# Kernel tuning notes

Measured on AMD Instinct MI355X. Metric: run time of the kernel, lower is better.

## Reference

```python
import jax, jax.numpy as jnp
import numpy as np

B, TU, TZ, V, H, E = 64, 128, 16, 32000, 512, 256
EPS = 1e-10


def setup_inputs() -> dict:
    key = jax.random.key(0)
    ks = jax.random.split(key, 22)
    s = 0.02  # weight init scale
    inp = {
        "embed_z": jax.random.normal(ks[0], (1, B, E), jnp.float32),
        "last_hidden": jax.random.normal(ks[1], (1, B, H), jnp.float32),
        "u_enc_out": jax.random.normal(ks[2], (TU, B, H), jnp.float32),
        # previous-turn z posterior: rows are probability distributions over vocab
        "pv_pz_proba": jax.nn.softmax(jax.random.normal(ks[3], (TZ, B, V), jnp.float32), axis=-1),
        "pv_z_dec_out": jax.random.normal(ks[4], (TZ, B, H), jnp.float32),
        "rand_eps": jax.random.normal(ks[5], (B, E), jnp.float32),
        "u_input_np": jax.random.randint(ks[6], (TU, B), 0, V),
        "u_input": jax.random.randint(ks[6], (TU, B), 0, V),   # unused by forward
        "m_input_np": jax.random.randint(ks[7], (TU, B), 0, V),  # unused by forward
        # GRU (single layer, single step)
        "W_ih": jax.random.normal(ks[8], (3 * H, E), jnp.float32) * s,
        "W_hh": jax.random.normal(ks[9], (3 * H, H), jnp.float32) * s,
        "b_ih": jnp.zeros((3 * H,), jnp.float32),
        "b_hh": jnp.zeros((3 * H,), jnp.float32),
        # w1: hidden -> vocab
        "W_w1": jax.random.normal(ks[10], (V, H), jnp.float32) * s,
        "b_w1": jnp.zeros((V,), jnp.float32),
        # proj_copy1 / proj_copy2: hidden -> hidden
        "W_p1": jax.random.normal(ks[11], (H, H), jnp.float32) * s,
        "b_p1": jnp.zeros((H,), jnp.float32),
        "W_p2": jax.random.normal(ks[12], (H, H), jnp.float32) * s,
        "b_p2": jnp.zeros((H,), jnp.float32),
        # mu / log_sigma: vocab -> embed
        "W_mu": jax.random.normal(ks[13], (E, V), jnp.float32) * s,
        "b_mu": jnp.zeros((E,), jnp.float32),
        "W_ls": jax.random.normal(ks[14], (E, V), jnp.float32) * s,
        "b_ls": jnp.zeros((E,), jnp.float32),
    }
    return inp


def reference(embed_z, last_hidden, u_enc_out, pv_pz_proba, pv_z_dec_out, rand_eps,
              u_input_np, u_input, m_input_np,
              W_ih, W_hh, b_ih, b_hh, W_w1, b_w1, W_p1, b_p1, W_p2, b_p2,
              W_mu, b_mu, W_ls, b_ls):
    # --- single GRU step (dropout is identity at rate 0 / eval) ---
    x = embed_z[0]          # (B,E)
    h0 = last_hidden[0]     # (B,H)
    gi = x @ W_ih.T + b_ih
    gh = h0 @ W_hh.T + b_hh
    i_r, i_z, i_n = jnp.split(gi, 3, axis=1)
    h_r, h_z, h_n = jnp.split(gh, 3, axis=1)
    r = jax.nn.sigmoid(i_r + h_r)
    z = jax.nn.sigmoid(i_z + h_z)
    n = jnp.tanh(i_n + r * h_n)
    h = (1.0 - z) * n + z * h0              # (B,H) == gru_out.squeeze(0)

    gen_score = h @ W_w1.T + b_w1           # (B,V)

    # --- user copy score (force_stable path): stable exp + scatter-add by token id ---
    uc = jnp.tanh(jnp.swapaxes(u_enc_out, 0, 1) @ W_p1.T + b_p1)   # (B,TU,H)
    us = jnp.einsum('bth,bh->bt', uc, h)                            # (B,TU)
    um = jnp.max(us, axis=1, keepdims=True)
    ue = jnp.exp(us - um)
    tok = u_input_np.T                                              # (B,TU)
    # sparse one-hot bmm == 1e-10 * sum_t e  +  scatter-add of e into vocab bin tok (tok!=0)
    scat = jnp.zeros((B, V), us.dtype).at[jnp.arange(B)[:, None], tok].add(
        ue * (tok != 0))
    u_copy = jnp.log(EPS * jnp.sum(ue, axis=1, keepdims=True) + scat) + um  # (B,V)

    # --- previous-z copy score (exp path taken when force_stable) ---
    # shift: drop last step, prepend 1e-10 fill
    shifted = jnp.concatenate(
        [jnp.full((1, B, V), EPS, pv_pz_proba.dtype), pv_pz_proba[:-1]], axis=0)  # (TZ,B,V)
    pc = jnp.tanh(jnp.swapaxes(pv_z_dec_out, 0, 1) @ W_p2.T + b_p2)  # (B,TZ,H)
    ps = jnp.exp(jnp.einsum('bth,bh->bt', pc, h))                    # (B,TZ)
    pv_copy = jnp.log(jnp.einsum('bt,tbv->bv', ps, shifted))         # (B,V)

    # --- joint softmax over [gen | u_copy | pv_copy], then merge ---
    scores = jax.nn.softmax(jnp.concatenate([gen_score, u_copy, pv_copy], axis=1), axis=1)
    g, u, p = jnp.split(scores, 3, axis=1)
    proba = g + u + p                        # (B,V)

    # --- VAE reparameterization ---
    appr_emb = proba @ W_mu.T + b_mu         # (B,E)
    log_sigma_ae = proba @ W_ls.T + b_ls
    sampled_ae = appr_emb + jnp.exp(log_sigma_ae) * rand_eps
    return sampled_ae, h[None], h[None], proba, appr_emb, log_sigma_ae
```

## Files before the change

### kernel.cpp

```cpp
#include <hip/hip_runtime.h>
#include <math.h>

#define B 64
#define TU 128
#define TZ 16
#define V 32000
#define H 512
#define E 256
#define EPSC 1e-10f

typedef __attribute__((ext_vector_type(8))) short bf16x8;
typedef __attribute__((ext_vector_type(4))) float f32x4;
#define MFMA16(a, b, c) __builtin_amdgcn_mfma_f32_16x16x32_bf16((a), (b), (c), 0, 0, 0)

union U8 { uint4 u; bf16x8 b; };

__device__ __forceinline__ unsigned short f2bf(float f) {
  unsigned u = __float_as_uint(f);
  u += 0x7FFFu + ((u >> 16) & 1u);
  return (unsigned short)(u >> 16);
}
__device__ __forceinline__ unsigned pack2(float a, float b) {
  return (unsigned)f2bf(a) | ((unsigned)f2bf(b) << 16);
}

__device__ __forceinline__ void stage64x512(unsigned short* __restrict__ dst,
                                            const unsigned short* __restrict__ src)
{
  const int tid = threadIdx.x;
#pragma unroll
  for (int j = 0; j < 16; ++j) {
    const int f = j * 256 + tid;
    const int s = f * 8;
    const int row = s >> 9, col = s & 511;
    *(uint4*)&dst[row * 520 + col] = *(const uint4*)&src[s];
  }
}

__device__ __forceinline__ void stage64x512_f32(unsigned short* __restrict__ dst,
                                                const float* __restrict__ src)
{
  const int tid = threadIdx.x;
#pragma unroll
  for (int j = 0; j < 16; ++j) {
    const int f = j * 256 + tid;
    const int s = f * 8;
    const int row = s >> 9, col = s & 511;
    float4 a = *(const float4*)&src[s];
    float4 b = *(const float4*)&src[s + 4];
    uint4 o;
    o.x = pack2(a.x, a.y); o.y = pack2(a.z, a.w);
    o.z = pack2(b.x, b.y); o.w = pack2(b.z, b.w);
    *(uint4*)&dst[row * 520 + col] = o;
  }
}

__device__ void gemm64_body(const float* __restrict__ A, int lda,
                            const float* __restrict__ Bm, int ldb,
                            const float* __restrict__ bias,
                            float* __restrict__ C, int ldc,
                            int iters, int nb)
{
  __shared__ float As[64][33];
  __shared__ float Bs[64][33];
  const int tid = threadIdx.x;
  const int n0 = nb * 64;
  const int tv = tid & 15, tb = tid >> 4;
  const int lr = tid >> 3;
  const int lc = (tid & 7) << 2;
  float acc[4][4] = {};

  for (int it = 0; it < iters; ++it) {
    const int kb = it * 32;
    float4 a0 = *(const float4*)&A[(size_t)lr * lda + kb + lc];
    float4 a1 = *(const float4*)&A[(size_t)(lr + 32) * lda + kb + lc];
    float4 b0 = *(const float4*)&Bm[(size_t)(n0 + lr) * ldb + kb + lc];
    float4 b1 = *(const float4*)&Bm[(size_t)(n0 + lr + 32) * ldb + kb + lc];
    __syncthreads();
    As[lr][lc] = a0.x; As[lr][lc + 1] = a0.y; As[lr][lc + 2] = a0.z; As[lr][lc + 3] = a0.w;
    As[lr + 32][lc] = a1.x; As[lr + 32][lc + 1] = a1.y; As[lr + 32][lc + 2] = a1.z; As[lr + 32][lc + 3] = a1.w;
    Bs[lr][lc] = b0.x; Bs[lr][lc + 1] = b0.y; Bs[lr][lc + 2] = b0.z; Bs[lr][lc + 3] = b0.w;
    Bs[lr + 32][lc] = b1.x; Bs[lr + 32][lc + 1] = b1.y; Bs[lr + 32][lc + 2] = b1.z; Bs[lr + 32][lc + 3] = b1.w;
    __syncthreads();
#pragma unroll
    for (int kk = 0; kk < 32; ++kk) {
      float av[4], bv[4];
#pragma unroll
      for (int i = 0; i < 4; ++i) av[i] = As[tb * 4 + i][kk];
#pragma unroll
      for (int j = 0; j < 4; ++j) bv[j] = Bs[tv * 4 + j][kk];
#pragma unroll
      for (int i = 0; i < 4; ++i)
#pragma unroll
        for (int j = 0; j < 4; ++j) acc[i][j] += av[i] * bv[j];
    }
  }
#pragma unroll
  for (int i = 0; i < 4; ++i)
#pragma unroll
    for (int j = 0; j < 4; ++j) {
      const int n = n0 + tv * 4 + j;
      C[(size_t)(tb * 4 + i) * ldc + n] = acc[i][j] + bias[n];
    }
}

__global__ __launch_bounds__(256) void k1_prep(
    float* __restrict__ zbuf,
    const float* __restrict__ embed_z, const float* __restrict__ W_ih,
    const float* __restrict__ b_ih, float* __restrict__ gi,
    const float* __restrict__ last_hid, const float* __restrict__ W_hh,
    const float* __restrict__ b_hh, float* __restrict__ gh)
{
  const int bx = blockIdx.x;
  if (bx == 0) {
    for (int i = threadIdx.x; i < 140352; i += 256) zbuf[i] = 0.f;
  } else if (bx < 25) {
    gemm64_body(embed_z, E, W_ih, E, b_ih, gi, 1536, 8, bx - 1);
  } else {
    gemm64_body(last_hid, H, W_hh, H, b_hh, gh, 1536, 16, bx - 25);
  }
}

__global__ void gru_gates(const float* __restrict__ gi, const float* __restrict__ gh,
                          const float* __restrict__ h0, float* __restrict__ h,
                          float* __restrict__ oh1, float* __restrict__ oh2,
                          unsigned short* __restrict__ hbf)
{
  const int b = blockIdx.x, k = threadIdx.x;
  const float ir = gi[b * 1536 + k], iz = gi[b * 1536 + 512 + k], in_ = gi[b * 1536 + 1024 + k];
  const float hr = gh[b * 1536 + k], hz = gh[b * 1536 + 512 + k], hn = gh[b * 1536 + 1024 + k];
  const float r = 1.f / (1.f + __expf(-(ir + hr)));
  const float z = 1.f / (1.f + __expf(-(iz + hz)));
  const float n = tanhf(in_ + r * hn);
  const float hv = (1.f - z) * n + z * h0[b * H + k];
  h[b * H + k] = hv;
  oh1[b * H + k] = hv;
  oh2[b * H + k] = hv;
  hbf[b * H + k] = f2bf(hv);
}

__device__ void us_body_f32(unsigned short* __restrict__ Ws,
                            const float* __restrict__ A,
                            const float* __restrict__ Wm,
                            const float* __restrict__ bias,
                            const float* __restrict__ hvec,
                            float* __restrict__ outp, int T, int m0, int n0)
{
  stage64x512_f32(Ws, Wm + (size_t)n0 * 512);
  __syncthreads();

  const int tid = threadIdx.x;
  const int wave = tid >> 6, lane = tid & 63;
  const int l15 = lane & 15, l4 = lane >> 4;
  const int mbase = m0 + wave * 32;
  const float* ga = A + (size_t)(mbase + l15) * 512 + l4 * 8;

  f32x4 acc[2][4];
#pragma unroll
  for (int i = 0; i < 2; ++i)
#pragma unroll
    for (int j = 0; j < 4; ++j) acc[i][j] = (f32x4)0.f;

#pragma unroll
  for (int it = 0; it < 16; ++it) {
    bf16x8 af[2], bf[4];
#pragma unroll
    for (int i = 0; i < 2; ++i) {
      float4 a0 = *(const float4*)(ga + (size_t)i * 16 * 512 + it * 32);
      float4 a1 = *(const float4*)(ga + (size_t)i * 16 * 512 + it * 32 + 4);
      U8 u;
      u.u.x = pack2(a0.x, a0.y); u.u.y = pack2(a0.z, a0.w);
      u.u.z = pack2(a1.x, a1.y); u.u.w = pack2(a1.z, a1.w);
      af[i] = u.b;
    }
#pragma unroll
    for (int j = 0; j < 4; ++j)
      bf[j] = *(const bf16x8*)&Ws[(j * 16 + l15) * 520 + it * 32 + l4 * 8];
#pragma unroll
    for (int i = 0; i < 2; ++i)
#pragma unroll
      for (int j = 0; j < 4; ++j) acc[i][j] = MFMA16(af[i], bf[j], acc[i][j]);
  }

#pragma unroll
  for (int i = 0; i < 2; ++i) {
#pragma unroll
    for (int q = 0; q < 4; ++q) {
      const int r = mbase + i * 16 + l4 * 4 + q;
      const int b = r & 63;
      float sum = 0.f;
#pragma unroll
      for (int j = 0; j < 4; ++j) {
        const int col = n0 + j * 16 + l15;
        const float x = acc[i][j][q] + bias[col];
        const float ex = __expf(2.f * x);
        const float th = 1.f - 2.f / (ex + 1.f);
        sum += th * hvec[b * H + col];
      }
      sum += __shfl_xor(sum, 1);
      sum += __shfl_xor(sum, 2);
      sum += __shfl_xor(sum, 4);
      sum += __shfl_xor(sum, 8);
      if (l15 == 0) atomicAdd(&outp[b * T + (r >> 6)], sum);
    }
  }
}

__global__ __launch_bounds__(256) void k23(
    const unsigned short* __restrict__ h_bf, const float* __restrict__ W_w1,
    const float* __restrict__ b_w1, float* __restrict__ num,
    const float* __restrict__ u_enc, const float* __restrict__ W_p1,
    const float* __restrict__ b_p1,
    const float* __restrict__ pv_zdec, const float* __restrict__ W_p2,
    const float* __restrict__ b_p2,
    const float* __restrict__ h, float* __restrict__ us, float* __restrict__ pcs)
{
  __shared__ unsigned short sh[64 * 520];
  const int bx = blockIdx.x;
  const int tid = threadIdx.x;
  const int wave = tid >> 6, lane = tid & 63;
  const int l15 = lane & 15, l4 = lane >> 4;

  if (bx < 500) {
    const int n0 = bx * 64;
    const int nrow = n0 + (wave << 4) + l15;
    const float* gw = W_w1 + (size_t)nrow * 512 + l4 * 8;

    float4 wv[32];
#pragma unroll
    for (int it = 0; it < 16; ++it) {
      wv[2 * it]     = *(const float4*)(gw + it * 32);
      wv[2 * it + 1] = *(const float4*)(gw + it * 32 + 4);
    }

    stage64x512(sh, h_bf);
    __syncthreads();

    f32x4 acc[4];
#pragma unroll
    for (int i = 0; i < 4; ++i) acc[i] = (f32x4)0.f;

#pragma unroll
    for (int it = 0; it < 16; ++it) {
      U8 u;
      u.u.x = pack2(wv[2 * it].x, wv[2 * it].y);
      u.u.y = pack2(wv[2 * it].z, wv[2 * it].w);
      u.u.z = pack2(wv[2 * it + 1].x, wv[2 * it + 1].y);
      u.u.w = pack2(wv[2 * it + 1].z, wv[2 * it + 1].w);
#pragma unroll
      for (int i = 0; i < 4; ++i) {
        bf16x8 af = *(const bf16x8*)&sh[(i * 16 + l15) * 520 + it * 32 + l4 * 8];
        acc[i] = MFMA16(af, u.b, acc[i]);
      }
    }

    const float bv = b_w1[nrow];
#pragma unroll
    for (int i = 0; i < 4; ++i)
#pragma unroll
      for (int q = 0; q < 4; ++q) {
        const int row = i * 16 + l4 * 4 + q;
        num[(size_t)row * V + nrow] = acc[i][q] + bv;
      }
  } else if (bx < 1012) {
    const int idx = bx - 500;
    const int xcd = idx & 7, loc = idx >> 3;
    const int m0 = (xcd * 8 + (loc & 7)) * 128;
    const int n0 = (loc >> 3) * 64;
    us_body_f32(sh, u_enc, W_p1, b_p1, h, us, TU, m0, n0);
  } else {
    const int idx = bx - 1012;
    const int m0 = (idx & 7) * 128;
    const int n0 = (idx >> 3) * 64;
    us_body_f32(sh, pv_zdec, W_p2, b_p2, h, pcs, TZ, m0, n0);
  }
}

__global__ void smalls_kernel(const float* __restrict__ us, const float* __restrict__ pcs,
                              float* __restrict__ ue, float* __restrict__ base,
                              float* __restrict__ Kb)
{
  const int b = blockIdx.x, t = threadIdx.x;
  __shared__ float sm[128];
  __shared__ float sK;
  const float u = us[b * TU + t];
  sm[t] = u; __syncthreads();
  for (int s = 64; s > 0; s >>= 1) {
    if (t < s) sm[t] = fmaxf(sm[t], sm[t + s]);
    __syncthreads();
  }
  if (t == 0) {
    float um = sm[0];
    float pm = -1e30f;
    for (int q = 0; q < TZ; ++q) pm = fmaxf(pm, pcs[b * TZ + q]);
    sK = fmaxf(fmaxf(um, pm), 0.0f);
  }
  __syncthreads();
  const float K = sK;
  const float e = __expf(u - K);
  ue[b * TU + t] = e;
  sm[t] = e; __syncthreads();
  for (int s = 64; s > 0; s >>= 1) {
    if (t < s) sm[t] += sm[t + s];
    __syncthreads();
  }
  if (t == 0) {
    Kb[b] = K;
    base[b] = EPSC * sm[0] + EPSC * __expf(pcs[b * TZ + 0] - K);
  }
}

__global__ __launch_bounds__(256) void fuse3(
    float* __restrict__ num, const float* __restrict__ pv,
    const float* __restrict__ pcs, const float* __restrict__ ue,
    const float* __restrict__ base, const float* __restrict__ Kb,
    const int* __restrict__ tok, float* __restrict__ Z,
    unsigned short* __restrict__ nb)
{
  __shared__ float elds[2000];
  __shared__ float red[256];
  const int bx = blockIdx.x, tid = threadIdx.x;
  const int b = bx >> 4, c = bx & 15;
  const float K = Kb[b];
  const float bs = base[b];
  float w[15];
#pragma unroll
  for (int s = 0; s < 15; ++s) w[s] = __expf(pcs[b * TZ + s + 1] - K);
  float4* nrow = (float4*)&num[(size_t)b * V];
  ushort4* brow = (ushort4*)&nb[(size_t)b * V];
  const float4* pv4 = (const float4*)pv;
  const int f0 = c * 500;
#pragma unroll
  for (int ji = 0; ji < 2; ++ji) {
    const int i = tid + ji * 256;
    if (i < 500) {
      float4 g = nrow[f0 + i];
      float4 e;
      e.x = __expf(g.x - K) + bs;
      e.y = __expf(g.y - K) + bs;
      e.z = __expf(g.z - K) + bs;
      e.w = __expf(g.w - K) + bs;
#pragma unroll
      for (int s = 0; s < 15; ++s) {
        const float4 f = pv4[(size_t)(s * B + b) * (V / 4) + f0 + i];
        e.x += w[s] * f.x; e.y += w[s] * f.y;
        e.z += w[s] * f.z; e.w += w[s] * f.w;
      }
      ((float4*)elds)[i] = e;
    }
  }
  __syncthreads();
  if (tid < TU) {
    const int tk = tok[tid * B + b];
    if (tk != 0) {
      const int lo = c * 2000;
      if (tk >= lo && tk < lo + 2000) atomicAdd(&elds[tk - lo], ue[b * TU + tid]);
    }
  }
  __syncthreads();
  float loc = 0.f;
#pragma unroll
  for (int ji = 0; ji < 2; ++ji) {
    const int i = tid + ji * 256;
    if (i < 500) {
      float4 e = ((float4*)elds)[i];
      nrow[f0 + i] = e;
      ushort4 o;
      o.x = f2bf(e.x); o.y = f2bf(e.y); o.z = f2bf(e.z); o.w = f2bf(e.w);
      brow[f0 + i] = o;
      loc += e.x + e.y + e.z + e.w;
    }
  }
  red[tid] = loc; __syncthreads();
  for (int st = 128; st > 0; st >>= 1) {
    if (tid < st) red[tid] += red[tid + st];
    __syncthreads();
  }
  if (tid == 0) atomicAdd(&Z[b], red[0]);
}

__global__ __launch_bounds__(256) void norm2(float* __restrict__ num,
                                             const float* __restrict__ Z)
{
  const int b = blockIdx.y;
  const int i4 = blockIdx.x * 256 + threadIdx.x;
  if (i4 >= V / 4) return;
  const float r = 1.0f / Z[b];
  float4* row = (float4*)&num[(size_t)b * V];
  float4 v = row[i4];
  v.x *= r; v.y *= r; v.z *= r; v.w *= r;
  row[i4] = v;
}

__global__ __launch_bounds__(256, 2) void k_muls(
    const unsigned short* __restrict__ Ab,
    const float* __restrict__ Wmu, const float* __restrict__ Wls,
    float* __restrict__ pmu, float* __restrict__ pls)
{
  const int tid = threadIdx.x;
  const int wave = tid >> 6, lane = tid & 63;
  const int l15 = lane & 15, l4 = lane >> 4;
  const float* gW = blockIdx.y ? Wls : Wmu;
  float* pO = (blockIdx.y ? pls : pmu) + (blockIdx.z & 3) * (B * E);
  const int kb0 = blockIdx.z * 128;
  const int c0 = blockIdx.x * 128 + wave * 32;

  const unsigned short* ga = Ab + (size_t)l15 * V + kb0 + l4 * 8;
  const float* gw0 = gW + (size_t)(c0 + l15) * V + kb0 + l4 * 8;
  const float* gw1 = gW + (size_t)(c0 + 16 + l15) * V + kb0 + l4 * 8;

  f32x4 acc[4][2];
#pragma unroll
  for (int i = 0; i < 4; ++i)
#pragma unroll
    for (int j = 0; j < 2; ++j) acc[i][j] = (f32x4)0.f;

#pragma unroll
  for (int it = 0; it < 4; ++it) {
    const int o = it * 32;
    bf16x8 af[4];
#pragma unroll
    for (int i = 0; i < 4; ++i)
      af[i] = *(const bf16x8*)(ga + (size_t)i * 16 * V + o);
    float4 a0 = *(const float4*)(gw0 + o), a1 = *(const float4*)(gw0 + o + 4);
    float4 b0 = *(const float4*)(gw1 + o), b1 = *(const float4*)(gw1 + o + 4);
    U8 u0, u1;
    u0.u.x = pack2(a0.x, a0.y); u0.u.y = pack2(a0.z, a0.w);
    u0.u.z = pack2(a1.x, a1.y); u0.u.w = pack2(a1.z, a1.w);
    u1.u.x = pack2(b0.x, b0.y); u1.u.y = pack2(b0.z, b0.w);
    u1.u.z = pack2(b1.x, b1.y); u1.u.w = pack2(b1.z, b1.w);
#pragma unroll
    for (int i = 0; i < 4; ++i) {
      acc[i][0] = MFMA16(af[i], u0.b, acc[i][0]);
      acc[i][1] = MFMA16(af[i], u1.b, acc[i][1]);
    }
  }
#pragma unroll
  for (int i = 0; i < 4; ++i)
#pragma unroll
    for (int j = 0; j < 2; ++j) {
      const int col = c0 + j * 16 + l15;
#pragma unroll
      for (int q = 0; q < 4; ++q) {
        const int row = i * 16 + l4 * 4 + q;
        atomicAdd(&pO[row * E + col], acc[i][j][q]);
      }
    }
}

__global__ void final2(const float* __restrict__ pmu, const float* __restrict__ pls,
                       const float* __restrict__ Z,
                       const float* __restrict__ bmu, const float* __restrict__ bls,
                       const float* __restrict__ eps_r, float* __restrict__ out)
{
  const int b = blockIdx.x, e = threadIdx.x;
  float smu = 0.f, sls = 0.f;
#pragma unroll
  for (int s = 0; s < 4; ++s) {
    smu += pmu[s * (B * E) + b * E + e];
    sls += pls[s * (B * E) + b * E + e];
  }
  const float rz = 1.0f / Z[b];
  const float ap = smu * rz + bmu[e];
  const float ls = sls * rz + bls[e];
  out[b * E + e] = ap + __expf(ls) * eps_r[b * E + e];
  out[2129920 + b * E + e] = ap;
  out[2146304 + b * E + e] = ls;
}

extern "C" void kernel_launch(void* const* d_in, const int* in_sizes, int n_in,
                              void* d_out_v, int out_size, void* d_ws, size_t ws_size,
                              hipStream_t stream)
{
  (void)in_sizes; (void)n_in; (void)out_size; (void)ws_size;
  const float* embed_z    = (const float*)d_in[0];
  const float* last_hid   = (const float*)d_in[1];
  const float* u_enc      = (const float*)d_in[2];
  const float* pv_pz      = (const float*)d_in[3];
  const float* pv_zdec    = (const float*)d_in[4];
  const float* rand_eps   = (const float*)d_in[5];
  const int*   u_input_np = (const int*)d_in[6];
  const float* W_ih = (const float*)d_in[9];
  const float* W_hh = (const float*)d_in[10];
  const float* b_ih = (const float*)d_in[11];
  const float* b_hh = (const float*)d_in[12];
  const float* W_w1 = (const float*)d_in[13];
  const float* b_w1 = (const float*)d_in[14];
  const float* W_p1 = (const float*)d_in[15];
  const float* b_p1 = (const float*)d_in[16];
  const float* W_p2 = (const float*)d_in[17];
  const float* b_p2 = (const float*)d_in[18];
  const float* W_mu = (const float*)d_in[19];
  const float* b_mu = (const float*)d_in[20];
  const float* W_ls = (const float*)d_in[21];
  const float* b_ls = (const float*)d_in[22];
  float* d_out = (float*)d_out_v;

  float* ws   = (float*)d_ws;
  float* h    = ws;
  float* gi   = ws + 32768;
  float* gh   = ws + 131072;
  float* us   = ws + 229376;
  float* pcs  = ws + 237568;
  float* Z    = ws + 238592;
  float* pmu  = ws + 238656;
  float* pls  = ws + 304192;
  float* ue   = ws + 369728;
  float* base = ws + 377920;
  float* Kb   = ws + 377984;
  unsigned short* h_bf   = (unsigned short*)(ws + 378048);
  unsigned short* num_bf = (unsigned short*)(ws + 394432);

  float* num   = d_out + 81920;
  float* outh1 = d_out + 16384;
  float* outh2 = d_out + 49152;

  k1_prep<<<dim3(49), 256, 0, stream>>>(
      us ,
      embed_z, W_ih, b_ih, gi, last_hid, W_hh, b_hh, gh);

  gru_gates<<<dim3(B), 512, 0, stream>>>(gi, gh, last_hid, h, outh1, outh2, h_bf);

  k23<<<dim3(1076), 256, 0, stream>>>(
      h_bf, W_w1, b_w1, num,
      u_enc, W_p1, b_p1,
      pv_zdec, W_p2, b_p2,
      h, us, pcs);

  smalls_kernel<<<dim3(B), 128, 0, stream>>>(us, pcs, ue, base, Kb);

  fuse3<<<dim3(1024), 256, 0, stream>>>(num, pv_pz, pcs, ue, base, Kb,
                                        u_input_np, Z, num_bf);

  k_muls<<<dim3(2, 2, 250), 256, 0, stream>>>(num_bf, W_mu, W_ls, pmu, pls);

  final2<<<dim3(B), 256, 0, stream>>>(pmu, pls, Z, b_mu, b_ls, rand_eps, d_out);

  norm2<<<dim3(32, B), 256, 0, stream>>>(num, Z);
}
```

Baseline: 170.3 us.

## Fold per-row max/exp stats into fuse3 and merge norm into k_muls launch

Removes the separate smalls_kernel by having every fuse3 block recompute the per-batch max K, exp(us-K) values and base term from us and pcs, and reuses the per-thread exp value directly for the scatter. It also eliminates the norm2 launch by appending its normalization blocks to the k_muls grid as extra block indices. This cuts two kernel launches and some workspace traffic, at the cost of 16x redundant small reductions per batch row and a flattened grid for k_muls.

```diff
diff --git a/kernel.cpp b/kernel.cpp
--- a/kernel.cpp
+++ b/kernel.cpp
@@ -276,53 +276,39 @@
   }
 }
 
-__global__ void smalls_kernel(const float* __restrict__ us, const float* __restrict__ pcs,
-                              float* __restrict__ ue, float* __restrict__ base,
-                              float* __restrict__ Kb)
-{
-  const int b = blockIdx.x, t = threadIdx.x;
-  __shared__ float sm[128];
+__global__ __launch_bounds__(256) void fuse3(
+    float* __restrict__ num, const float* __restrict__ pv,
+    const float* __restrict__ pcs, const float* __restrict__ us,
+    const int* __restrict__ tok, float* __restrict__ Z,
+    unsigned short* __restrict__ nb)
+{
+  __shared__ float elds[2000];
+  __shared__ float red[256];
   __shared__ float sK;
-  const float u = us[b * TU + t];
-  sm[t] = u; __syncthreads();
-  for (int s = 64; s > 0; s >>= 1) {
-    if (t < s) sm[t] = fmaxf(sm[t], sm[t + s]);
+  const int bx = blockIdx.x, tid = threadIdx.x;
+  const int b = bx >> 4, c = bx & 15;
+
+  float m = (tid < TU) ? us[b * TU + tid] : -1e30f;
+  red[tid] = m; __syncthreads();
+  for (int s = 128; s > 0; s >>= 1) {
+    if (tid < s) red[tid] = fmaxf(red[tid], red[tid + s]);
     __syncthreads();
   }
-  if (t == 0) {
-    float um = sm[0];
+  if (tid == 0) {
     float pm = -1e30f;
     for (int q = 0; q < TZ; ++q) pm = fmaxf(pm, pcs[b * TZ + q]);
-    sK = fmaxf(fmaxf(um, pm), 0.0f);
+    sK = fmaxf(fmaxf(red[0], pm), 0.0f);
   }
   __syncthreads();
   const float K = sK;
-  const float e = __expf(u - K);
-  ue[b * TU + t] = e;
-  sm[t] = e; __syncthreads();
-  for (int s = 64; s > 0; s >>= 1) {
-    if (t < s) sm[t] += sm[t + s];
+  float e_t = (tid < TU) ? __expf(us[b * TU + tid] - K) : 0.f;
+  red[tid] = e_t; __syncthreads();
+  for (int s = 128; s > 0; s >>= 1) {
+    if (tid < s) red[tid] += red[tid + s];
     __syncthreads();
   }
-  if (t == 0) {
-    Kb[b] = K;
-    base[b] = EPSC * sm[0] + EPSC * __expf(pcs[b * TZ + 0] - K);
-  }
-}
-
-__global__ __launch_bounds__(256) void fuse3(
-    float* __restrict__ num, const float* __restrict__ pv,
-    const float* __restrict__ pcs, const float* __restrict__ ue,
-    const float* __restrict__ base, const float* __restrict__ Kb,
-    const int* __restrict__ tok, float* __restrict__ Z,
-    unsigned short* __restrict__ nb)
-{
-  __shared__ float elds[2000];
-  __shared__ float red[256];
-  const int bx = blockIdx.x, tid = threadIdx.x;
-  const int b = bx >> 4, c = bx & 15;
-  const float K = Kb[b];
-  const float bs = base[b];
+  const float bs = EPSC * red[0] + EPSC * __expf(pcs[b * TZ] - K);
+
   float w[15];
 #pragma unroll
   for (int s = 0; s < 15; ++s) w[s] = __expf(pcs[b * TZ + s + 1] - K);
@@ -354,7 +340,7 @@
     const int tk = tok[tid * B + b];
     if (tk != 0) {
       const int lo = c * 2000;
-      if (tk >= lo && tk < lo + 2000) atomicAdd(&elds[tk - lo], ue[b * TU + tid]);
+      if (tk >= lo && tk < lo + 2000) atomicAdd(&elds[tk - lo], e_t);
     }
   }
   __syncthreads();
@@ -379,73 +365,76 @@
   if (tid == 0) atomicAdd(&Z[b], red[0]);
 }
 
-__global__ __launch_bounds__(256) void norm2(float* __restrict__ num,
-                                             const float* __restrict__ Z)
-{
-  const int b = blockIdx.y;
-  const int i4 = blockIdx.x * 256 + threadIdx.x;
-  if (i4 >= V / 4) return;
-  const float r = 1.0f / Z[b];
-  float4* row = (float4*)&num[(size_t)b * V];
-  float4 v = row[i4];
-  v.x *= r; v.y *= r; v.z *= r; v.w *= r;
-  row[i4] = v;
-}
-
 __global__ __launch_bounds__(256, 2) void k_muls(
     const unsigned short* __restrict__ Ab,
     const float* __restrict__ Wmu, const float* __restrict__ Wls,
-    float* __restrict__ pmu, float* __restrict__ pls)
-{
+    float* __restrict__ pmu, float* __restrict__ pls,
+    float* __restrict__ num, const float* __restrict__ Z)
+{
+  const int bx = blockIdx.x;
   const int tid = threadIdx.x;
-  const int wave = tid >> 6, lane = tid & 63;
-  const int l15 = lane & 15, l4 = lane >> 4;
-  const float* gW = blockIdx.y ? Wls : Wmu;
-  float* pO = (blockIdx.y ? pls : pmu) + (blockIdx.z & 3) * (B * E);
-  const int kb0 = blockIdx.z * 128;
-  const int c0 = blockIdx.x * 128 + wave * 32;
-
-  const unsigned short* ga = Ab + (size_t)l15 * V + kb0 + l4 * 8;
-  const float* gw0 = gW + (size_t)(c0 + l15) * V + kb0 + l4 * 8;
-  const float* gw1 = gW + (size_t)(c0 + 16 + l15) * V + kb0 + l4 * 8;
-
-  f32x4 acc[4][2];
-#pragma unroll
-  for (int i = 0; i < 4; ++i)
-#pragma unroll
-    for (int j = 0; j < 2; ++j) acc[i][j] = (f32x4)0.f;
-
-#pragma unroll
-  for (int it = 0; it < 4; ++it) {
-    const int o = it * 32;
-    bf16x8 af[4];
+  if (bx < 1000) {
+    const int x = bx & 1, y = (bx >> 1) & 1, z = bx >> 2;
+    const int wave = tid >> 6, lane = tid & 63;
+    const int l15 = lane & 15, l4 = lane >> 4;
+    const float* gW = y ? Wls : Wmu;
+    float* pO = (y ? pls : pmu) + (z & 3) * (B * E);
+    const int kb0 = z * 128;
+    const int c0 = x * 128 + wave * 32;
+
+    const unsigned short* ga = Ab + (size_t)l15 * V + kb0 + l4 * 8;
+    const float* gw0 = gW + (size_t)(c0 + l15) * V + kb0 + l4 * 8;
+    const float* gw1 = gW + (size_t)(c0 + 16 + l15) * V + kb0 + l4 * 8;
+
+    f32x4 acc[4][2];
 #pragma unroll
     for (int i = 0; i < 4; ++i)
-      af[i] = *(const bf16x8*)(ga + (size_t)i * 16 * V + o);
-    float4 a0 = *(const float4*)(gw0 + o), a1 = *(const float4*)(gw0 + o + 4);
-    float4 b0 = *(const float4*)(gw1 + o), b1 = *(const float4*)(gw1 + o + 4);
-    U8 u0, u1;
-    u0.u.x = pack2(a0.x, a0.y); u0.u.y = pack2(a0.z, a0.w);
-    u0.u.z = pack2(a1.x, a1.y); u0.u.w = pack2(a1.z, a1.w);
-    u1.u.x = pack2(b0.x, b0.y); u1.u.y = pack2(b0.z, b0.w);
-    u1.u.z = pack2(b1.x, b1.y); u1.u.w = pack2(b1.z, b1.w);
-#pragma unroll
-    for (int i = 0; i < 4; ++i) {
-      acc[i][0] = MFMA16(af[i], u0.b, acc[i][0]);
-      acc[i][1] = MFMA16(af[i], u1.b, acc[i][1]);
-    }
-  }
-#pragma unroll
-  for (int i = 0; i < 4; ++i)
-#pragma unroll
-    for (int j = 0; j < 2; ++j) {
-      const int col = c0 + j * 16 + l15;
-#pragma unroll
-      for (int q = 0; q < 4; ++q) {
-        const int row = i * 16 + l4 * 4 + q;
-        atomicAdd(&pO[row * E + col], acc[i][j][q]);
+#pragma unroll
+      for (int j = 0; j < 2; ++j) acc[i][j] = (f32x4)0.f;
+
+#pragma unroll
+    for (int it = 0; it < 4; ++it) {
+      const int o = it * 32;
+      bf16x8 af[4];
+#pragma unroll
+      for (int i = 0; i < 4; ++i)
+        af[i] = *(const bf16x8*)(ga + (size_t)i * 16 * V + o);
+      float4 a0 = *(const float4*)(gw0 + o), a1 = *(const float4*)(gw0 + o + 4);
+      float4 b0 = *(const float4*)(gw1 + o), b1 = *(const float4*)(gw1 + o + 4);
+      U8 u0, u1;
+      u0.u.x = pack2(a0.x, a0.y); u0.u.y = pack2(a0.z, a0.w);
+      u0.u.z = pack2(a1.x, a1.y); u0.u.w = pack2(a1.z, a1.w);
+      u1.u.x = pack2(b0.x, b0.y); u1.u.y = pack2(b0.z, b0.w);
+      u1.u.z = pack2(b1.x, b1.y); u1.u.w = pack2(b1.z, b1.w);
+#pragma unroll
+      for (int i = 0; i < 4; ++i) {
+        acc[i][0] = MFMA16(af[i], u0.b, acc[i][0]);
+        acc[i][1] = MFMA16(af[i], u1.b, acc[i][1]);
       }
     }
+#pragma unroll
+    for (int i = 0; i < 4; ++i)
+#pragma unroll
+      for (int j = 0; j < 2; ++j) {
+        const int col = c0 + j * 16 + l15;
+#pragma unroll
+        for (int q = 0; q < 4; ++q) {
+          const int row = i * 16 + l4 * 4 + q;
+          atomicAdd(&pO[row * E + col], acc[i][j][q]);
+        }
+      }
+  } else {
+    const int idx = bx - 1000;
+    const int b = idx >> 5;
+    const int i4 = (idx & 31) * 256 + tid;
+    if (i4 < V / 4) {
+      const float r = 1.0f / Z[b];
+      float4* row = (float4*)&num[(size_t)b * V];
+      float4 v = row[i4];
+      v.x *= r; v.y *= r; v.z *= r; v.w *= r;
+      row[i4] = v;
+    }
+  }
 }
 
 __global__ void final2(const float* __restrict__ pmu, const float* __restrict__ pls,
@@ -505,11 +494,8 @@
   float* Z    = ws + 238592;
   float* pmu  = ws + 238656;
   float* pls  = ws + 304192;
-  float* ue   = ws + 369728;
-  float* base = ws + 377920;
-  float* Kb   = ws + 377984;
-  unsigned short* h_bf   = (unsigned short*)(ws + 378048);
-  unsigned short* num_bf = (unsigned short*)(ws + 394432);
+  unsigned short* h_bf   = (unsigned short*)(ws + 369728);
+  unsigned short* num_bf = (unsigned short*)(ws + 386112);
 
   float* num   = d_out + 81920;
   float* outh1 = d_out + 16384;
@@ -527,14 +513,10 @@
       pv_zdec, W_p2, b_p2,
       h, us, pcs);
 
-  smalls_kernel<<<dim3(B), 128, 0, stream>>>(us, pcs, ue, base, Kb);
-
-  fuse3<<<dim3(1024), 256, 0, stream>>>(num, pv_pz, pcs, ue, base, Kb,
+  fuse3<<<dim3(1024), 256, 0, stream>>>(num, pv_pz, pcs, us,
                                         u_input_np, Z, num_bf);
 
-  k_muls<<<dim3(2, 2, 250), 256, 0, stream>>>(num_bf, W_mu, W_ls, pmu, pls);
+  k_muls<<<dim3(3048), 256, 0, stream>>>(num_bf, W_mu, W_ls, pmu, pls, num, Z);
 
   final2<<<dim3(B), 256, 0, stream>>>(pmu, pls, Z, b_mu, b_ls, rand_eps, d_out);
-
-  norm2<<<dim3(32, B), 256, 0, stream>>>(num, Z);
-}
+}
```

Measured after the change: 166.2 us. -2.4%, faster.
